# Kernel optimization log

Measured on AMD Instinct MI355X. Metric: run time of the kernel, lower is better.

## Reference

```python
import itertools
import jax, jax.numpy as jnp
import numpy as np


def _interpn_linear(vol, loc):
    """Trilinear sampling with edge-clamping (voxelmorph interpn, fill_value=None).
    vol: [D, H, W, C] float; loc: [D, H, W, 3] float absolute sample coordinates (ij indexing).
    """
    spatial = vol.shape[:-1]
    ndims = len(spatial)
    maxs = jnp.asarray([s - 1 for s in spatial], dtype=loc.dtype)
    cloc = jnp.clip(loc, 0.0, maxs)             # clamp = nearest-neighbor fill outside domain
    loc0 = jnp.floor(cloc)
    loc1 = jnp.minimum(loc0 + 1.0, maxs)
    d1 = loc1 - cloc                            # weight for the low corner (loc0)
    d0 = 1.0 - d1                               # weight for the high corner (loc1)
    loc0i = loc0.astype(jnp.int32)
    loc1i = loc1.astype(jnp.int32)

    # flatten volume and build per-dim strides for linear indexing
    volf = vol.reshape(-1, vol.shape[-1])       # [D*H*W, C]
    strides = np.ones(ndims, dtype=np.int32)
    for d in range(ndims - 2, -1, -1):
        strides[d] = strides[d + 1] * spatial[d + 1]

    out = jnp.zeros(spatial + (vol.shape[-1],), dtype=vol.dtype)
    for corner in itertools.product((0, 1), repeat=ndims):
        idx = jnp.zeros(spatial, dtype=jnp.int32)
        w = jnp.ones(spatial, dtype=vol.dtype)
        for d in range(ndims):
            idx = idx + (loc1i if corner[d] else loc0i)[..., d] * strides[d]
            w = w * (d0 if corner[d] else d1)[..., d]
        out = out + w[..., None] * jnp.take(volf, idx, axis=0)
    return out


def _warp_single(vol, disp):
    """Apply dense displacement field: sample vol at identity grid + disp."""
    spatial = vol.shape[:-1]
    grid = jnp.stack(
        jnp.meshgrid(*[jnp.arange(s, dtype=disp.dtype) for s in spatial], indexing='ij'),
        axis=-1)                                # [D, H, W, 3]
    return _interpn_linear(vol, grid + disp)


def setup_inputs() -> dict:
    key = jax.random.key(0)
    k1, k2 = jax.random.split(key)
    vol = jax.random.normal(k1, (2, 128, 192, 192, 1), dtype=jnp.float32)
    trf = jax.random.normal(k2, (2, 128, 192, 192, 3), dtype=jnp.float32)
    return {"vol": vol, "trf": trf}


def reference(vol, trf):
    # batched dense-warp spatial transformer (single_transform=False)
    return jax.vmap(_warp_single)(vol, trf)
```

## Files before the change

### kernel.cpp

```cpp
#include <hip/hip_runtime.h>
#include <stdint.h>


#define BD 128
#define BH 192
#define BW 192
#define DHW (BD*BH*BW)
#define NB 2

#define TX 16
#define TY 16
#define TZ 8
#define NTX (BW/TX)
#define NTY (BH/TY)
#define NTZ (BD/TZ)
#define NBLK (NTX*NTY*NTZ*NB)
#define NXCD 8

#define SXW 25
#define SYW 24
#define SZW 16
#define SLAB (SXW*SYW)
#define LDSF (SLAB*SZW)

typedef float f4v __attribute__((ext_vector_type(4)));

__global__ __launch_bounds__(256, 4) void st_warp_kernel(
    const float* __restrict__ vol,
    const float* __restrict__ trf,
    float* __restrict__ out)
{
    __shared__ float lds[LDSF + 4];

    const int bid = blockIdx.x;
    const int swz = (bid % NXCD) * (NBLK / NXCD) + bid / NXCD;
    int tmp = swz;
    const int txi = tmp % NTX; tmp /= NTX;
    const int tyi = tmp % NTY; tmp /= NTY;
    const int tzi = tmp % NTZ; tmp /= NTZ;
    const int b   = tmp;
    const int tx = txi*TX, ty = tyi*TY, tz = tzi*TZ;

    const int sx = min(max(tx - 4, 0), BW - SXW);
    const int sy = min(max(ty - 4, 0), BH - SYW);
    const int sz = min(max(tz - 4, 0), BD - SZW);

    const int tid = (int)threadIdx.x;
    const float* volb = vol + (size_t)b * DHW;

#pragma unroll
    for (int it = 0; it < 38; ++it) {
        const int p = tid + it*256;
        if (p < LDSF) {
            const int zi  = p / SLAB;
            const int rem = p - zi*SLAB;
            const int yi  = rem / SXW;
            const int xi  = rem - yi*SXW;
            const float* g = volb + ((size_t)((sz+zi)*BH + (sy+yi)))*BW + sx + xi;
            __builtin_amdgcn_global_load_lds(
                (const __attribute__((address_space(1))) void*)g,
                (__attribute__((address_space(3))) void*)&lds[p],
                4, 0, 0);
        }
    }
    if (tid < 4) lds[LDSF + tid] = 0.0f;

    const f4v* trf4 = (const f4v*)trf;
    f4v tA[2], tB[2], tC[2];
#pragma unroll
    for (int i = 0; i < 2; ++i) {
        const int gi = i*256 + tid;
        const int xq = gi & 3;
        const int yb = (gi >> 2) & 15;
        const int zb = gi >> 6;
        const size_t rowf4 = ((size_t)((b*BD + tz+zb)*BH + ty+yb)*BW + tx) * 3 / 4;
        tA[i] = trf4[rowf4 + 3*xq + 0];
        tB[i] = trf4[rowf4 + 3*xq + 1];
        tC[i] = trf4[rowf4 + 3*xq + 2];
    }

    __syncthreads();

#pragma unroll
    for (int i = 0; i < 2; ++i) {
        const float dzs[4] = {tA[i].x, tA[i].w, tB[i].z, tC[i].y};
        const float dys[4] = {tA[i].y, tB[i].x, tB[i].w, tC[i].z};
        const float dxs[4] = {tA[i].z, tB[i].y, tC[i].x, tC[i].w};
        const int gi = i*256 + tid;
        const int xq = gi & 3;
        const int yb = (gi >> 2) & 15;
        const int zb = gi >> 6;
        const int Y  = ty + yb;
        const int Z  = tz + zb;
        const int Xb = tx + xq*4;
        float res[4];
#pragma unroll
        for (int jj = 0; jj < 4; ++jj) {
            float cz = fminf(fmaxf((float)Z + dzs[jj], 0.f), (float)(BD-1));
            float cy = fminf(fmaxf((float)Y + dys[jj], 0.f), (float)(BH-1));
            float cx = fminf(fmaxf((float)(Xb+jj) + dxs[jj], 0.f), (float)(BW-1));
            float fz = floorf(cz), fy = floorf(cy), fx = floorf(cx);
            int z0 = (int)fz, y0 = (int)fy, x0 = (int)fx;
            int z1 = min(z0+1, BD-1);
            int y1 = min(y0+1, BH-1);
            int x1 = min(x0+1, BW-1);
            float wz = cz - fz, wy = cy - fy, wx = cx - fx;
            float v000,v001,v010,v011,v100,v101,v110,v111;
            bool inwin = (x0 >= sx) & (x1 <= sx+SXW-1) & (y0 >= sy) & (y1 <= sy+SYW-1)
                       & (z0 >= sz) & (z1 <= sz+SZW-1);
            if (inwin) {
                const int zi0 = z0 - sz, zi1 = z1 - sz;
                const int yi0 = y0 - sy, yi1 = y1 - sy;
                const int xi  = x0 - sx;
                const int i00 = zi0*SLAB + yi0*SXW + xi;
                const int i01 = zi0*SLAB + yi1*SXW + xi;
                const int i10 = zi1*SLAB + yi0*SXW + xi;
                const int i11 = zi1*SLAB + yi1*SXW + xi;
                v000 = lds[i00]; v001 = lds[i00+1];
                v010 = lds[i01]; v011 = lds[i01+1];
                v100 = lds[i10]; v101 = lds[i10+1];
                v110 = lds[i11]; v111 = lds[i11+1];
            } else {
                const float* p00 = volb + ((size_t)z0*BH + y0)*BW;
                const float* p01 = volb + ((size_t)z0*BH + y1)*BW;
                const float* p10 = volb + ((size_t)z1*BH + y0)*BW;
                const float* p11 = volb + ((size_t)z1*BH + y1)*BW;
                v000 = p00[x0]; v001 = p00[x1];
                v010 = p01[x0]; v011 = p01[x1];
                v100 = p10[x0]; v101 = p10[x1];
                v110 = p11[x0]; v111 = p11[x1];
            }
            float c00 = v000 + wx*(v001-v000);
            float c01 = v010 + wx*(v011-v010);
            float c10 = v100 + wx*(v101-v100);
            float c11 = v110 + wx*(v111-v110);
            float c0  = c00 + wy*(c01-c00);
            float c1  = c10 + wy*(c11-c10);
            res[jj]   = c0 + wz*(c1-c0);
        }
        f4v r = {res[0], res[1], res[2], res[3]};
        const size_t of4 = ((size_t)((b*BD + Z)*BH + Y)*BW + Xb) / 4;
        __builtin_nontemporal_store(r, &((f4v*)out)[of4]);
    }
}

extern "C" void kernel_launch(void* const* d_in, const int* in_sizes, int n_in,
                              void* d_out, int out_size, void* d_ws, size_t ws_size,
                              hipStream_t stream) {
    const float* vol = (const float*)d_in[0];
    const float* trf = (const float*)d_in[1];
    float* out = (float*)d_out;

    st_warp_kernel<<<dim3(NBLK), dim3(256), 0, stream>>>(vol, trf, out);
}
```

Measured before the change: 51.48 us.

## Halve tile height, shrink LDS halo window, raise occupancy to 6 blocks

Shrinks the output tile from 16x16x8 to 16x8x8 so each thread handles one 4-voxel group, and cuts the LDS window's y extent from 24 to 16, which reduces LDS use and lets launch bounds request 6 blocks per CU. The staging loop now covers the window exactly in 25 iterations, using a multiply-shift divide and no bounds check. The nontemporal output store becomes a plain store. The trade-off is a higher halo-to-interior ratio, so more displaced samples may fall outside the window and take the slower global-load fallback, and the grid has twice as many blocks.

```diff
diff --git a/kernel.cpp b/kernel.cpp
--- a/kernel.cpp
+++ b/kernel.cpp
@@ -9,7 +9,7 @@
 #define NB 2
 
 #define TX 16
-#define TY 16
+#define TY 8
 #define TZ 8
 #define NTX (BW/TX)
 #define NTY (BH/TY)
@@ -18,14 +18,14 @@
 #define NXCD 8
 
 #define SXW 25
-#define SYW 24
+#define SYW 16
 #define SZW 16
 #define SLAB (SXW*SYW)
 #define LDSF (SLAB*SZW)
 
 typedef float f4v __attribute__((ext_vector_type(4)));
 
-__global__ __launch_bounds__(256, 4) void st_warp_kernel(
+__global__ __launch_bounds__(256, 6) void st_warp_kernel(
     const float* __restrict__ vol,
     const float* __restrict__ trf,
     float* __restrict__ out)
@@ -49,99 +49,85 @@
     const float* volb = vol + (size_t)b * DHW;
 
 #pragma unroll
-    for (int it = 0; it < 38; ++it) {
-        const int p = tid + it*256;
-        if (p < LDSF) {
-            const int zi  = p / SLAB;
-            const int rem = p - zi*SLAB;
-            const int yi  = rem / SXW;
-            const int xi  = rem - yi*SXW;
-            const float* g = volb + ((size_t)((sz+zi)*BH + (sy+yi)))*BW + sx + xi;
-            __builtin_amdgcn_global_load_lds(
-                (const __attribute__((address_space(1))) void*)g,
-                (__attribute__((address_space(3))) void*)&lds[p],
-                4, 0, 0);
-        }
+    for (int it = 0; it < 25; ++it) {
+        const int p  = tid + it*256;
+        const int ri = (int)(((unsigned)p * 5243u) >> 17);
+        const int xi = p - ri*25;
+        const int zi = ri >> 4;
+        const int yi = ri & 15;
+        const float* g = volb + ((size_t)((sz+zi)*BH + (sy+yi)))*BW + sx + xi;
+        __builtin_amdgcn_global_load_lds(
+            (const __attribute__((address_space(1))) void*)g,
+            (__attribute__((address_space(3))) void*)&lds[p],
+            4, 0, 0);
     }
     if (tid < 4) lds[LDSF + tid] = 0.0f;
 
+    const int xq = tid & 3;
+    const int yb = (tid >> 2) & 7;
+    const int zb = tid >> 5;
+    const int Y  = ty + yb;
+    const int Z  = tz + zb;
+    const int Xb = tx + xq*4;
     const f4v* trf4 = (const f4v*)trf;
-    f4v tA[2], tB[2], tC[2];
-#pragma unroll
-    for (int i = 0; i < 2; ++i) {
-        const int gi = i*256 + tid;
-        const int xq = gi & 3;
-        const int yb = (gi >> 2) & 15;
-        const int zb = gi >> 6;
-        const size_t rowf4 = ((size_t)((b*BD + tz+zb)*BH + ty+yb)*BW + tx) * 3 / 4;
-        tA[i] = trf4[rowf4 + 3*xq + 0];
-        tB[i] = trf4[rowf4 + 3*xq + 1];
-        tC[i] = trf4[rowf4 + 3*xq + 2];
-    }
+    const size_t rowf4 = ((size_t)((b*BD + Z)*BH + Y)*BW + tx) * 3 / 4;
+    const f4v tA = trf4[rowf4 + 3*xq + 0];
+    const f4v tB = trf4[rowf4 + 3*xq + 1];
+    const f4v tC = trf4[rowf4 + 3*xq + 2];
 
     __syncthreads();
 
+    const float dzs[4] = {tA.x, tA.w, tB.z, tC.y};
+    const float dys[4] = {tA.y, tB.x, tB.w, tC.z};
+    const float dxs[4] = {tA.z, tB.y, tC.x, tC.w};
+    float res[4];
 #pragma unroll
-    for (int i = 0; i < 2; ++i) {
-        const float dzs[4] = {tA[i].x, tA[i].w, tB[i].z, tC[i].y};
-        const float dys[4] = {tA[i].y, tB[i].x, tB[i].w, tC[i].z};
-        const float dxs[4] = {tA[i].z, tB[i].y, tC[i].x, tC[i].w};
-        const int gi = i*256 + tid;
-        const int xq = gi & 3;
-        const int yb = (gi >> 2) & 15;
-        const int zb = gi >> 6;
-        const int Y  = ty + yb;
-        const int Z  = tz + zb;
-        const int Xb = tx + xq*4;
-        float res[4];
-#pragma unroll
-        for (int jj = 0; jj < 4; ++jj) {
-            float cz = fminf(fmaxf((float)Z + dzs[jj], 0.f), (float)(BD-1));
-            float cy = fminf(fmaxf((float)Y + dys[jj], 0.f), (float)(BH-1));
-            float cx = fminf(fmaxf((float)(Xb+jj) + dxs[jj], 0.f), (float)(BW-1));
-            float fz = floorf(cz), fy = floorf(cy), fx = floorf(cx);
-            int z0 = (int)fz, y0 = (int)fy, x0 = (int)fx;
-            int z1 = min(z0+1, BD-1);
-            int y1 = min(y0+1, BH-1);
-            int x1 = min(x0+1, BW-1);
-            float wz = cz - fz, wy = cy - fy, wx = cx - fx;
-            float v000,v001,v010,v011,v100,v101,v110,v111;
-            bool inwin = (x0 >= sx) & (x1 <= sx+SXW-1) & (y0 >= sy) & (y1 <= sy+SYW-1)
-                       & (z0 >= sz) & (z1 <= sz+SZW-1);
-            if (inwin) {
-                const int zi0 = z0 - sz, zi1 = z1 - sz;
-                const int yi0 = y0 - sy, yi1 = y1 - sy;
-                const int xi  = x0 - sx;
-                const int i00 = zi0*SLAB + yi0*SXW + xi;
-                const int i01 = zi0*SLAB + yi1*SXW + xi;
-                const int i10 = zi1*SLAB + yi0*SXW + xi;
-                const int i11 = zi1*SLAB + yi1*SXW + xi;
-                v000 = lds[i00]; v001 = lds[i00+1];
-                v010 = lds[i01]; v011 = lds[i01+1];
-                v100 = lds[i10]; v101 = lds[i10+1];
-                v110 = lds[i11]; v111 = lds[i11+1];
-            } else {
-                const float* p00 = volb + ((size_t)z0*BH + y0)*BW;
-                const float* p01 = volb + ((size_t)z0*BH + y1)*BW;
-                const float* p10 = volb + ((size_t)z1*BH + y0)*BW;
-                const float* p11 = volb + ((size_t)z1*BH + y1)*BW;
-                v000 = p00[x0]; v001 = p00[x1];
-                v010 = p01[x0]; v011 = p01[x1];
-                v100 = p10[x0]; v101 = p10[x1];
-                v110 = p11[x0]; v111 = p11[x1];
-            }
-            float c00 = v000 + wx*(v001-v000);
-            float c01 = v010 + wx*(v011-v010);
-            float c10 = v100 + wx*(v101-v100);
-            float c11 = v110 + wx*(v111-v110);
-            float c0  = c00 + wy*(c01-c00);
-            float c1  = c10 + wy*(c11-c10);
-            res[jj]   = c0 + wz*(c1-c0);
+    for (int jj = 0; jj < 4; ++jj) {
+        float cz = fminf(fmaxf((float)Z + dzs[jj], 0.f), (float)(BD-1));
+        float cy = fminf(fmaxf((float)Y + dys[jj], 0.f), (float)(BH-1));
+        float cx = fminf(fmaxf((float)(Xb+jj) + dxs[jj], 0.f), (float)(BW-1));
+        float fz = floorf(cz), fy = floorf(cy), fx = floorf(cx);
+        int z0 = (int)fz, y0 = (int)fy, x0 = (int)fx;
+        int z1 = min(z0+1, BD-1);
+        int y1 = min(y0+1, BH-1);
+        int x1 = min(x0+1, BW-1);
+        float wz = cz - fz, wy = cy - fy, wx = cx - fx;
+        float v000,v001,v010,v011,v100,v101,v110,v111;
+        bool inwin = (x0 >= sx) & (x1 <= sx+SXW-1) & (y0 >= sy) & (y1 <= sy+SYW-1)
+                   & (z0 >= sz) & (z1 <= sz+SZW-1);
+        if (inwin) {
+            const int zi0 = z0 - sz, zi1 = z1 - sz;
+            const int yi0 = y0 - sy, yi1 = y1 - sy;
+            const int xi  = x0 - sx;
+            const int i00 = zi0*SLAB + yi0*SXW + xi;
+            const int i01 = zi0*SLAB + yi1*SXW + xi;
+            const int i10 = zi1*SLAB + yi0*SXW + xi;
+            const int i11 = zi1*SLAB + yi1*SXW + xi;
+            v000 = lds[i00]; v001 = lds[i00+1];
+            v010 = lds[i01]; v011 = lds[i01+1];
+            v100 = lds[i10]; v101 = lds[i10+1];
+            v110 = lds[i11]; v111 = lds[i11+1];
+        } else {
+            const float* p00 = volb + ((size_t)z0*BH + y0)*BW;
+            const float* p01 = volb + ((size_t)z0*BH + y1)*BW;
+            const float* p10 = volb + ((size_t)z1*BH + y0)*BW;
+            const float* p11 = volb + ((size_t)z1*BH + y1)*BW;
+            v000 = p00[x0]; v001 = p00[x1];
+            v010 = p01[x0]; v011 = p01[x1];
+            v100 = p10[x0]; v101 = p10[x1];
+            v110 = p11[x0]; v111 = p11[x1];
         }
-        f4v r = {res[0], res[1], res[2], res[3]};
-        const size_t of4 = ((size_t)((b*BD + Z)*BH + Y)*BW + Xb) / 4;
-        __builtin_nontemporal_store(r, &((f4v*)out)[of4]);
+        float c00 = v000 + wx*(v001-v000);
+        float c01 = v010 + wx*(v011-v010);
+        float c10 = v100 + wx*(v101-v100);
+        float c11 = v110 + wx*(v111-v110);
+        float c0  = c00 + wy*(c01-c00);
+        float c1  = c10 + wy*(c11-c10);
+        res[jj]   = c0 + wz*(c1-c0);
     }
+    f4v r = {res[0], res[1], res[2], res[3]};
+    const size_t of4 = ((size_t)((b*BD + Z)*BH + Y)*BW + Xb) / 4;
+    ((f4v*)out)[of4] = r;
 }
 
 extern "C" void kernel_launch(void* const* d_in, const int* in_sizes, int n_in,
```

Measured after the change: 61.58 us. 1.2x slower.
